# Optimization experiments

Measured on AMD Instinct MI355X. Metric: run time of the kernel, lower is better.

Reference implementation:

```python
import jax, jax.numpy as jnp
import numpy as np
import math

HIDDEN = 1024
HEADS = 16
HEAD_DIM = HIDDEN // HEADS


def setup_inputs() -> dict:
    key = jax.random.key(0)
    ks = jax.random.split(key, 9)
    B, T, C = 4, 2048, HIDDEN
    s = 0.02
    x = jax.random.normal(ks[0], (B, T, C), dtype=jnp.float32)
    # torch nn.Linear weights are [out_features, in_features]
    Wq = jax.random.normal(ks[1], (C, C), dtype=jnp.float32) * s
    Wk = jax.random.normal(ks[2], (C, C), dtype=jnp.float32) * s
    Wv = jax.random.normal(ks[3], (C, C), dtype=jnp.float32) * s
    Wo = jax.random.normal(ks[4], (C, C), dtype=jnp.float32) * s
    bq = jax.random.normal(ks[5], (C,), dtype=jnp.float32) * s
    bk = jax.random.normal(ks[6], (C,), dtype=jnp.float32) * s
    bv = jax.random.normal(ks[7], (C,), dtype=jnp.float32) * s
    bo = jax.random.normal(ks[8], (C,), dtype=jnp.float32) * s
    return {"x": x, "Wq": Wq, "bq": bq, "Wk": Wk, "bk": bk,
            "Wv": Wv, "bv": bv, "Wo": Wo, "bo": bo}


def reference(x, Wq, bq, Wk, bk, Wv, bv, Wo, bo):
    B, T, C = x.shape
    H, D = HEADS, HEAD_DIM
    # projections: torch Linear => x @ W.T + b
    q = (x @ Wq.T + bq).reshape(B, T, H, D).transpose(0, 2, 1, 3)  # [B,H,T,D]
    k = (x @ Wk.T + bk).reshape(B, T, H, D).transpose(0, 2, 1, 3)
    v = (x @ Wv.T + bv).reshape(B, T, H, D).transpose(0, 2, 1, 3)
    scale = 1.0 / math.sqrt(D)
    scores = jnp.einsum('bhqd,bhkd->bhqk', q, k) * scale  # [B,H,T,T]
    attn = jax.nn.softmax(scores, axis=-1)
    y = jnp.einsum('bhqk,bhkd->bhqd', attn, v)  # [B,H,T,D]
    y = y.transpose(0, 2, 1, 3).reshape(B, T, C)
    return y @ Wo.T + bo
```

## Files before the change

kernel.cpp:

```cpp
#include <hip/hip_runtime.h>
#include <stdint.h>


using u16 = unsigned short;
using u32 = unsigned int;
typedef __attribute__((ext_vector_type(8))) __bf16 bf16x8;
typedef __attribute__((ext_vector_type(4))) float  floatx4;

#define QSCALE 0.18033688011112043f

__device__ __forceinline__ u16 f2b(float f) {
    union { float f; u32 i; } x; x.f = f;
    return (u16)((x.i + 0x7fffu + ((x.i >> 16) & 1u)) >> 16);
}
__device__ __forceinline__ u32 fbits(float f) { union { float f; u32 i; } x; x.f = f; return x.i; }
__device__ __forceinline__ u32 pkbf(float a, float b) {
    u32 ia = fbits(a) + 0x8000u, ib = fbits(b) + 0x8000u;
    return __builtin_amdgcn_perm(ib, ia, 0x07060302u);
}
__device__ __forceinline__ bf16x8 ld16B(const u16* p) {
    bf16x8 v; __builtin_memcpy(&v, p, 16); return v;
}
__device__ __forceinline__ void async16(const u16* g, u16* l) {
    __builtin_amdgcn_global_load_lds((const __attribute__((address_space(1))) unsigned int*)g,
                                     (__attribute__((address_space(3))) unsigned int*)l,
                                     16, 0, 0);
}

__global__ __launch_bounds__(256) void convert_kernel(
    const float* __restrict__ x,
    const float* __restrict__ Wq, const float* __restrict__ Wk,
    const float* __restrict__ Wv, const float* __restrict__ Wo,
    u16* __restrict__ xb, u16* __restrict__ wqb, u16* __restrict__ wkb,
    u16* __restrict__ wvb, u16* __restrict__ wob)
{
    size_t e = ((size_t)blockIdx.x * 256 + threadIdx.x) * 4;
    const float* src; u16* dst; size_t off;
    const size_t XN = (size_t)8 << 20;
    if (e < XN) { src = x; dst = xb; off = e; }
    else {
        size_t k = e - XN;
        int w = (int)(k >> 20);
        off = k & ((1u << 20) - 1);
        src = (w == 0) ? Wq : (w == 1) ? Wk : (w == 2) ? Wv : Wo;
        dst = (w == 0) ? wqb : (w == 1) ? wkb : (w == 2) ? wvb : wob;
    }
    float4 f = *(const float4*)(src + off);
    u32 dws[2] = { pkbf(f.x, f.y), pkbf(f.z, f.w) };
    __builtin_memcpy(dst + off, dws, 8);
}

__device__ __forceinline__ void gemm_loop(const u16* __restrict__ A, const u16* __restrict__ W,
                                          int m0, int n0, floatx4 (&acc)[4][4],
                                          u16* __restrict__ sA, u16* __restrict__ sB)
{
    constexpr int K = 1024;
    const int tid  = threadIdx.x;
    const int wave = tid >> 6, lane = tid & 63;
    const int wr = wave >> 1, wc = wave & 1;
    const int quad = lane >> 4, l15 = lane & 15;

    #pragma unroll
    for (int i = 0; i < 4; ++i)
        #pragma unroll
        for (int j = 0; j < 4; ++j)
            acc[i][j] = (floatx4){0.f, 0.f, 0.f, 0.f};

    const int rstage = lane >> 3;
    const int gstage = lane & 7;

    #pragma unroll
    for (int j = 0; j < 4; ++j) {
        int r  = wave * 32 + j * 8 + rstage;
        int kg = gstage ^ (r & 7);
        async16(A + (size_t)(m0 + r) * K + kg * 8, &sA[(wave * 32 + j * 8) * 64]);
        async16(W + (size_t)(n0 + r) * K + kg * 8, &sB[(wave * 32 + j * 8) * 64]);
    }
    __syncthreads();

    #pragma unroll 1
    for (int kb = 0; kb < 16; ++kb) {
        const int cur = kb & 1;
        if (kb < 15) {
            const int k0 = (kb + 1) * 64;
            u16* dA = sA + (cur ^ 1) * 8192;
            u16* dB = sB + (cur ^ 1) * 8192;
            #pragma unroll
            for (int j = 0; j < 4; ++j) {
                int r  = wave * 32 + j * 8 + rstage;
                int kg = gstage ^ (r & 7);
                async16(A + (size_t)(m0 + r) * K + k0 + kg * 8, &dA[(wave * 32 + j * 8) * 64]);
                async16(W + (size_t)(n0 + r) * K + k0 + kg * 8, &dB[(wave * 32 + j * 8) * 64]);
            }
        }
        const u16* bA = sA + cur * 8192;
        const u16* bB = sB + cur * 8192;

        #pragma unroll
        for (int kk = 0; kk < 2; ++kk) {
            bf16x8 af[4], bf[4];
            const int kg = kk * 4 + quad;
            #pragma unroll
            for (int t = 0; t < 4; ++t) {
                int ra = wr * 64 + t * 16 + l15;
                af[t] = ld16B(&bA[ra * 64 + ((kg ^ (ra & 7)) * 8)]);
                int rb = wc * 64 + t * 16 + l15;
                bf[t] = ld16B(&bB[rb * 64 + ((kg ^ (rb & 7)) * 8)]);
            }
            #pragma unroll
            for (int mt = 0; mt < 4; ++mt)
                #pragma unroll
                for (int nt = 0; nt < 4; ++nt)
                    acc[mt][nt] = __builtin_amdgcn_mfma_f32_16x16x32_bf16(af[mt], bf[nt], acc[mt][nt], 0, 0, 0);
        }
        __syncthreads();
    }
}

__global__ __launch_bounds__(256, 2) void qkv_kernel(
    const u16* __restrict__ x, const u16* __restrict__ Wcat,
    const float* __restrict__ bq, const float* __restrict__ bk, const float* __restrict__ bv,
    u16* __restrict__ q, u16* __restrict__ k, u16* __restrict__ vt)
{
    __shared__ __align__(16) u16 sA[2 * 128 * 64];
    __shared__ __align__(16) u16 sB[2 * 128 * 64];
    const int m0 = blockIdx.y * 128, n0 = blockIdx.x * 128;
    floatx4 acc[4][4];
    gemm_loop(x, Wcat, m0, n0, acc, sA, sB);

    const int tid = threadIdx.x;
    const int wave = tid >> 6, lane = tid & 63;
    const int wr = wave >> 1, wc = wave & 1;
    const int quad = lane >> 4, l15 = lane & 15;

    const int z = n0 >> 10;
    const float* bb = (z == 0) ? bq : (z == 1) ? bk : bv;
    const float scale = (z == 0) ? QSCALE : 1.0f;
    u16* o = (z == 0) ? q : k;

    #pragma unroll
    for (int nt = 0; nt < 4; ++nt) {
        int col  = n0 + wc * 64 + nt * 16 + l15;
        int c    = col & 1023;
        float bv_ = bb[c];
        #pragma unroll
        for (int mt = 0; mt < 4; ++mt) {
            int row0 = m0 + wr * 64 + mt * 16 + quad * 4;
            if (z == 2) {
                float v0 = acc[mt][nt][0] + bv_, v1 = acc[mt][nt][1] + bv_;
                float v2 = acc[mt][nt][2] + bv_, v3 = acc[mt][nt][3] + bv_;
                u32 dws[2] = { pkbf(v0, v1), pkbf(v2, v3) };
                int b = row0 >> 11, t0 = row0 & 2047;
                size_t idx = ((size_t)((b * 16 + (c >> 6)) * 64 + (c & 63)) * 2048) + t0;
                __builtin_memcpy(vt + idx, dws, 8);
            } else {
                #pragma unroll
                for (int r = 0; r < 4; ++r) {
                    float v = (acc[mt][nt][r] + bv_) * scale;
                    o[(size_t)(row0 + r) * 1024 + c] = f2b(v);
                }
            }
        }
    }
}

__global__ __launch_bounds__(256, 2) void proj_kernel(
    const u16* __restrict__ y, const u16* __restrict__ Wo, const float* __restrict__ bo,
    float* __restrict__ out)
{
    __shared__ __align__(16) u16 sA[2 * 128 * 64];
    __shared__ __align__(16) u16 sB[2 * 128 * 64];
    const int m0 = blockIdx.y * 128, n0 = blockIdx.x * 128;
    floatx4 acc[4][4];
    gemm_loop(y, Wo, m0, n0, acc, sA, sB);

    const int tid = threadIdx.x;
    const int wave = tid >> 6, lane = tid & 63;
    const int wr = wave >> 1, wc = wave & 1;
    const int quad = lane >> 4, l15 = lane & 15;

    #pragma unroll
    for (int nt = 0; nt < 4; ++nt) {
        int col = n0 + wc * 64 + nt * 16 + l15;
        float bv_ = bo[col];
        #pragma unroll
        for (int mt = 0; mt < 4; ++mt) {
            int row0 = m0 + wr * 64 + mt * 16 + quad * 4;
            #pragma unroll
            for (int r = 0; r < 4; ++r)
                out[(size_t)(row0 + r) * 1024 + col] = acc[mt][nt][r] + bv_;
        }
    }
}

__global__ __launch_bounds__(256, 2) void attn_kernel(
    const u16* __restrict__ Q, const u16* __restrict__ K,
    const u16* __restrict__ Vt, u16* __restrict__ Y)
{
    const int bh = blockIdx.x, qt = blockIdx.y;
    const int tid = threadIdx.x;
    const int wave = tid >> 6, lane = tid & 63;
    const int quad = lane >> 4, l15 = lane & 15, l7 = l15 & 7;
    const int b = bh >> 4, h = bh & 15;

    __shared__ __align__(16) u16 sK[2][64 * 64];
    __shared__ __align__(16) u16 sP[4][64 * 72];

    const __bf16 one = (__bf16)1.0f;
    const bf16x8 ones = { one, one, one, one, one, one, one, one };

    bf16x8 qf[4][2];
    #pragma unroll
    for (int nt = 0; nt < 4; ++nt) {
        const u16* qp = Q + (size_t)(b * 2048 + qt * 256 + wave * 64 + nt * 16 + l15) * 1024 + h * 64 + quad * 8;
        qf[nt][0] = ld16B(qp);
        qf[nt][1] = ld16B(qp + 32);
    }

    const int r8 = lane >> 3;
    const int g7 = (lane & 7) ^ r8;
    const u16* ksrc = K + (size_t)(b * 2048 + wave * 16 + r8) * 1024 + h * 64 + g7 * 8;
    const u16* vbase = Vt + (size_t)(bh * 64) * 2048;

    floatx4 accO[4][4];
    #pragma unroll
    for (int mt = 0; mt < 4; ++mt)
        #pragma unroll
        for (int nt = 0; nt < 4; ++nt) accO[mt][nt] = (floatx4){0.f, 0.f, 0.f, 0.f};
    floatx4 accR[4];
    #pragma unroll
    for (int nt = 0; nt < 4; ++nt) accR[nt] = (floatx4){0.f, 0.f, 0.f, 0.f};

    {
        u16* dK = &sK[0][wave * 16 * 64];
        async16(ksrc,            dK);
        async16(ksrc + 8 * 1024, dK + 8 * 64);
    }
    __syncthreads();

    u16* sp = sP[wave];
    const int spRow = l15 * 72;

    #pragma unroll 1
    for (int kt = 0; kt < 32; ++kt) {
        const int cur = kt & 1;
        if (kt < 31) {
            u16* dK = &sK[cur ^ 1][wave * 16 * 64];
            const u16* ks = ksrc + (size_t)(kt + 1) * 64 * 1024;
            async16(ks,            dK);
            async16(ks + 8 * 1024, dK + 8 * 64);
        }
        bf16x8 vf[4][2];
        #pragma unroll
        for (int mt = 0; mt < 4; ++mt)
            #pragma unroll
            for (int kk = 0; kk < 2; ++kk)
                vf[mt][kk] = ld16B(vbase + (size_t)(mt * 16 + l15) * 2048 + kt * 64 + (kk * 4 + quad) * 8);

        const u16* bK = sK[cur];
        bf16x8 kf[4][2];
        #pragma unroll
        for (int mt = 0; mt < 4; ++mt)
            #pragma unroll
            for (int kk = 0; kk < 2; ++kk)
                kf[mt][kk] = ld16B(&bK[(mt * 16 + l15) * 64 + (((kk * 4 + quad) ^ l7) * 8)]);

        #pragma unroll
        for (int nt = 0; nt < 4; ++nt) {
            floatx4 st[4];
            #pragma unroll
            for (int mt = 0; mt < 4; ++mt) st[mt] = (floatx4){0.f, 0.f, 0.f, 0.f};
            #pragma unroll
            for (int kk = 0; kk < 2; ++kk)
                #pragma unroll
                for (int mt = 0; mt < 4; ++mt)
                    st[mt] = __builtin_amdgcn_mfma_f32_16x16x32_bf16(kf[mt][kk], qf[nt][kk], st[mt], 0, 0, 0);

            u16* spn = sp + nt * 16 * 72 + spRow;
            #pragma unroll
            for (int mt = 0; mt < 4; ++mt) {
                float p0 = __builtin_amdgcn_exp2f(st[mt][0]);
                float p1 = __builtin_amdgcn_exp2f(st[mt][1]);
                float p2 = __builtin_amdgcn_exp2f(st[mt][2]);
                float p3 = __builtin_amdgcn_exp2f(st[mt][3]);
                u32 dws[2] = { pkbf(p0, p1), pkbf(p2, p3) };
                __builtin_memcpy(spn + mt * 16 + quad * 4, dws, 8);
            }
            bf16x8 pf0 = ld16B(spn + quad * 8);
            bf16x8 pf1 = ld16B(spn + 32 + quad * 8);
            accR[nt] = __builtin_amdgcn_mfma_f32_16x16x32_bf16(ones, pf0, accR[nt], 0, 0, 0);
            accR[nt] = __builtin_amdgcn_mfma_f32_16x16x32_bf16(ones, pf1, accR[nt], 0, 0, 0);
            #pragma unroll
            for (int mt = 0; mt < 4; ++mt) {
                accO[mt][nt] = __builtin_amdgcn_mfma_f32_16x16x32_bf16(vf[mt][0], pf0, accO[mt][nt], 0, 0, 0);
                accO[mt][nt] = __builtin_amdgcn_mfma_f32_16x16x32_bf16(vf[mt][1], pf1, accO[mt][nt], 0, 0, 0);
            }
        }
        __syncthreads();
    }

    float inv[4];
    #pragma unroll
    for (int nt = 0; nt < 4; ++nt) inv[nt] = 1.f / accR[nt][0];
    #pragma unroll
    for (int nt = 0; nt < 4; ++nt)
        #pragma unroll
        for (int mt = 0; mt < 4; ++mt) {
            u32 dws[2] = { pkbf(accO[mt][nt][0] * inv[nt], accO[mt][nt][1] * inv[nt]),
                           pkbf(accO[mt][nt][2] * inv[nt], accO[mt][nt][3] * inv[nt]) };
            __builtin_memcpy(&sp[(nt * 16 + l15) * 72 + mt * 16 + quad * 4], dws, 8);
        }
    const int rl = lane >> 3, cl = lane & 7;
    #pragma unroll
    for (int pass = 0; pass < 8; ++pass) {
        int qq = pass * 8 + rl;
        int t = qt * 256 + wave * 64 + qq;
        bf16x8 vrow = ld16B(&sp[qq * 72 + cl * 8]);
        __builtin_memcpy(Y + ((size_t)(b * 2048 + t)) * 1024 + h * 64 + cl * 8, &vrow, 16);
    }
}

extern "C" void kernel_launch(void* const* d_in, const int* in_sizes, int n_in,
                              void* d_out, int out_size, void* d_ws, size_t ws_size,
                              hipStream_t stream)
{
    const float* x  = (const float*)d_in[0];
    const float* Wq = (const float*)d_in[1];
    const float* bq = (const float*)d_in[2];
    const float* Wk = (const float*)d_in[3];
    const float* bk = (const float*)d_in[4];
    const float* Wv = (const float*)d_in[5];
    const float* bv = (const float*)d_in[6];
    const float* Wo = (const float*)d_in[7];
    const float* bo = (const float*)d_in[8];
    float* out = (float*)d_out;

    const size_t NTOK = (size_t)8192 * 1024;
    const size_t WN   = (size_t)1024 * 1024;
    u16* xb  = (u16*)d_ws;
    u16* wqb = xb + NTOK;
    u16* wkb = wqb + WN;
    u16* wvb = wkb + WN;
    u16* wob = wvb + WN;
    u16* q   = wob + WN;
    u16* k   = q + NTOK;
    u16* vt  = k + NTOK;
    u16* y   = vt + NTOK;

    convert_kernel<<<dim3(12288), 256, 0, stream>>>(x, Wq, Wk, Wv, Wo, xb, wqb, wkb, wvb, wob);
    qkv_kernel<<<dim3(24, 64), 256, 0, stream>>>(xb, wqb, bq, bk, bv, q, k, vt);
    attn_kernel<<<dim3(64, 8), 256, 0, stream>>>(q, k, vt, y);
    proj_kernel<<<dim3(8, 64), 256, 0, stream>>>(y, wob, bo, out);
}
```

Baseline: 274.6 us.

## Stage V tiles through LDS asynchronously and remap GEMM blocks per XCD

The attention kernel now double-buffers V^T tiles into shared memory with async global-to-LDS loads, prefetched alongside K, instead of reading V fragments straight from global memory each iteration. This hides V load latency at the cost of extra LDS. The QKV and output-projection GEMMs switch to a 1D grid whose block index is remapped so that blocks landing on the same XCD share row tiles, aiming for better L2 reuse.

Measured after the change: 261.4 us. -4.8%, faster.

```diff
diff --git a/kernel.cpp b/kernel.cpp
--- a/kernel.cpp
+++ b/kernel.cpp
@@ -124,7 +124,10 @@
 {
     __shared__ __align__(16) u16 sA[2 * 128 * 64];
     __shared__ __align__(16) u16 sB[2 * 128 * 64];
-    const int m0 = blockIdx.y * 128, n0 = blockIdx.x * 128;
+    const int id = blockIdx.x;
+    const int xcd = id & 7, slot = id >> 3;
+    const int m0 = (xcd * 8 + (slot & 7)) * 128;
+    const int n0 = (slot >> 3) * 128;
     floatx4 acc[4][4];
     gemm_loop(x, Wcat, m0, n0, acc, sA, sB);
 
@@ -170,7 +173,10 @@
 {
     __shared__ __align__(16) u16 sA[2 * 128 * 64];
     __shared__ __align__(16) u16 sB[2 * 128 * 64];
-    const int m0 = blockIdx.y * 128, n0 = blockIdx.x * 128;
+    const int id = blockIdx.x;
+    const int xcd = id & 7, slot = id >> 3;
+    const int m0 = (xcd * 8 + (slot & 7)) * 128;
+    const int n0 = (slot >> 3) * 128;
     floatx4 acc[4][4];
     gemm_loop(y, Wo, m0, n0, acc, sA, sB);
 
@@ -204,6 +210,7 @@
     const int b = bh >> 4, h = bh & 15;
 
     __shared__ __align__(16) u16 sK[2][64 * 64];
+    __shared__ __align__(16) u16 sV[2][64 * 64];
     __shared__ __align__(16) u16 sP[4][64 * 72];
 
     const __bf16 one = (__bf16)1.0f;
@@ -219,8 +226,8 @@
 
     const int r8 = lane >> 3;
     const int g7 = (lane & 7) ^ r8;
-    const u16* ksrc = K + (size_t)(b * 2048 + wave * 16 + r8) * 1024 + h * 64 + g7 * 8;
-    const u16* vbase = Vt + (size_t)(bh * 64) * 2048;
+    const u16* ksrc = K  + (size_t)(b * 2048 + wave * 16 + r8) * 1024 + h * 64 + g7 * 8;
+    const u16* vsrc = Vt + ((size_t)(bh * 64 + wave * 16 + r8)) * 2048 + g7 * 8;
 
     floatx4 accO[4][4];
     #pragma unroll
@@ -233,8 +240,11 @@
 
     {
         u16* dK = &sK[0][wave * 16 * 64];
+        u16* dV = &sV[0][wave * 16 * 64];
         async16(ksrc,            dK);
         async16(ksrc + 8 * 1024, dK + 8 * 64);
+        async16(vsrc,            dV);
+        async16(vsrc + 8 * 2048, dV + 8 * 64);
     }
     __syncthreads();
 
@@ -246,24 +256,25 @@
         const int cur = kt & 1;
         if (kt < 31) {
             u16* dK = &sK[cur ^ 1][wave * 16 * 64];
+            u16* dV = &sV[cur ^ 1][wave * 16 * 64];
             const u16* ks = ksrc + (size_t)(kt + 1) * 64 * 1024;
+            const u16* vs = vsrc + (size_t)(kt + 1) * 64;
             async16(ks,            dK);
             async16(ks + 8 * 1024, dK + 8 * 64);
-        }
-        bf16x8 vf[4][2];
+            async16(vs,            dV);
+            async16(vs + 8 * 2048, dV + 8 * 64);
+        }
+        const u16* bK = sK[cur];
+        const u16* bV = sV[cur];
+
+        bf16x8 kf[4][2], vf[4][2];
         #pragma unroll
         for (int mt = 0; mt < 4; ++mt)
             #pragma unroll
-            for (int kk = 0; kk < 2; ++kk)
-                vf[mt][kk] = ld16B(vbase + (size_t)(mt * 16 + l15) * 2048 + kt * 64 + (kk * 4 + quad) * 8);
-
-        const u16* bK = sK[cur];
-        bf16x8 kf[4][2];
-        #pragma unroll
-        for (int mt = 0; mt < 4; ++mt)
-            #pragma unroll
-            for (int kk = 0; kk < 2; ++kk)
+            for (int kk = 0; kk < 2; ++kk) {
                 kf[mt][kk] = ld16B(&bK[(mt * 16 + l15) * 64 + (((kk * 4 + quad) ^ l7) * 8)]);
+                vf[mt][kk] = ld16B(&bV[(mt * 16 + l15) * 64 + (((kk * 4 + quad) ^ l7) * 8)]);
+            }
 
         #pragma unroll
         for (int nt = 0; nt < 4; ++nt) {
@@ -348,7 +359,7 @@
     u16* y   = vt + NTOK;
 
     convert_kernel<<<dim3(12288), 256, 0, stream>>>(x, Wq, Wk, Wv, Wo, xb, wqb, wkb, wvb, wob);
-    qkv_kernel<<<dim3(24, 64), 256, 0, stream>>>(xb, wqb, bq, bk, bv, q, k, vt);
+    qkv_kernel<<<dim3(1536), 256, 0, stream>>>(xb, wqb, bq, bk, bv, q, k, vt);
     attn_kernel<<<dim3(64, 8), 256, 0, stream>>>(q, k, vt, y);
-    proj_kernel<<<dim3(8, 64), 256, 0, stream>>>(y, wob, bo, out);
-}
+    proj_kernel<<<dim3(512), 256, 0, stream>>>(y, wob, bo, out);
+}
```
